# Performance work log

Measured on AMD Instinct MI355X. Metric: run time of the kernel, lower is better.

## Reference

```python
import jax, jax.numpy as jnp
import numpy as np

NUM_HEADS = 16

def setup_inputs() -> dict:
    key = jax.random.key(0)
    ks = jax.random.split(key, 12)
    B, NQ, NK = 4, 1024, 1024
    DQ = DK = DV = 1024
    AH = 1024   # num_heads * head_dim
    OUT = 1024
    s = lambda d: 1.0 / np.sqrt(d)
    return {
        "q": jax.random.normal(ks[0], (B, NQ, DQ), jnp.float32),
        "k": jax.random.normal(ks[1], (B, NK, DK), jnp.float32),
        "v": jax.random.normal(ks[2], (B, NK, DV), jnp.float32),
        "attn_mask": jnp.ones((NQ, NK), jnp.float32),
        "Wq": jax.random.normal(ks[3], (DQ, AH), jnp.float32) * s(DQ),
        "bq": jnp.zeros((AH,), jnp.float32),
        "Wk": jax.random.normal(ks[4], (DK, AH), jnp.float32) * s(DK),
        "bk": jnp.zeros((AH,), jnp.float32),
        "Wv": jax.random.normal(ks[5], (DV, AH), jnp.float32) * s(DV),
        "bv": jnp.zeros((AH,), jnp.float32),
        "Wo": jax.random.normal(ks[6], (AH, OUT), jnp.float32) * s(AH),
        "bo": jnp.zeros((OUT,), jnp.float32),
    }

def reference(q, k, v, attn_mask, Wq, bq, Wk, bk, Wv, bv, Wo, bo):
    b, n_q, _ = q.shape
    n_k = k.shape[1]
    all_head_dim = Wq.shape[1]
    scale = all_head_dim ** (-0.5)  # NOTE: module scales by all_head_dim, not head_dim

    # module reshapes as (b, n, head_dim, num_heads): heads are the LAST axis
    def split_heads(x):
        return x.reshape(b, x.shape[1], -1, NUM_HEADS).transpose(0, 3, 1, 2)  # (b,H,n,d)

    qh = split_heads(q @ Wq + bq) * scale
    kh = split_heads(k @ Wk + bk)
    vh = split_heads(v @ Wv + bv)

    attn = jnp.einsum('bhqd,bhkd->bhqk', qh, kh)
    attn = attn - 100000000.0 * (1.0 - attn_mask[None, None, :, :])
    attn = jax.nn.softmax(attn, axis=-1)

    o = jnp.einsum('bhqk,bhkd->bhqd', attn, vh)
    o = o.transpose(0, 2, 3, 1).reshape(b, n_q, -1)  # (b,n_q,head_dim*H)
    return o @ Wo + bo
```

## Files before the change

### kernel.cpp

```cpp
#include <hip/hip_runtime.h>
#include <stdint.h>

typedef __attribute__((ext_vector_type(8))) short short8;
typedef __attribute__((ext_vector_type(8))) unsigned short ushort8;
typedef __attribute__((ext_vector_type(4))) float f32x4;
typedef unsigned short u16;
typedef unsigned int u32;

__device__ __forceinline__ u16 f2bf(float f){
  u32 u = __builtin_bit_cast(u32, f);
  u32 r = (u + 0x7fffu + ((u >> 16) & 1u)) >> 16;
  return (u16)r;
}

__device__ __forceinline__ void gload16(const void* g, void* l){
  __builtin_amdgcn_global_load_lds((const __attribute__((address_space(1))) void*)g,
                                   (__attribute__((address_space(3))) void*)l, 16, 0, 0);
}

__global__ void cast3_kernel(const float* __restrict__ q, const float* __restrict__ k,
                             const float* __restrict__ v, u16* __restrict__ xq,
                             u16* __restrict__ xk, u16* __restrict__ xv){
  const int NV8 = 4194304 / 8;
  int stride = gridDim.x * blockDim.x;
  for (int i = blockIdx.x * blockDim.x + threadIdx.x; i < 3 * NV8; i += stride){
    int t = i / NV8, r = i - t * NV8;
    const float4* src = (const float4*)(t == 0 ? q : (t == 1 ? k : v));
    u16* dst = (t == 0 ? xq : (t == 1 ? xk : xv));
    float4 f0 = src[r * 2], f1 = src[r * 2 + 1];
    ushort8 o;
    o[0] = f2bf(f0.x); o[1] = f2bf(f0.y); o[2] = f2bf(f0.z); o[3] = f2bf(f0.w);
    o[4] = f2bf(f1.x); o[5] = f2bf(f1.y); o[6] = f2bf(f1.z); o[7] = f2bf(f1.w);
    *(ushort8*)(dst + r * 8) = o;
  }
}

__global__ void transw_kernel(const float* __restrict__ Wq, const float* __restrict__ Wk,
                              const float* __restrict__ Wv, const float* __restrict__ Wo,
                              u16* __restrict__ WqT, u16* __restrict__ WkT,
                              u16* __restrict__ WvT, u16* __restrict__ WoT){
  __shared__ float t[64][65];
  int z = blockIdx.z;
  const float* src = (z == 0 ? Wq : (z == 1 ? Wk : (z == 2 ? Wv : Wo)));
  u16* dst = (z == 0 ? WqT : (z == 1 ? WkT : (z == 2 ? WvT : WoT)));
  int tid = threadIdx.x;
  int bx = blockIdx.x, by = blockIdx.y;
  int c0 = by * 64;
  #pragma unroll
  for (int p = 0; p < 4; ++p){
    int rl = p * 16 + (tid >> 4);
    int srcRow = (z < 3) ? (bx * 64 + rl) : (rl * 16 + bx);
    float4 f = *(const float4*)(src + srcRow * 1024 + c0 + (tid & 15) * 4);
    t[rl][(tid & 15) * 4 + 0] = f.x;
    t[rl][(tid & 15) * 4 + 1] = f.y;
    t[rl][(tid & 15) * 4 + 2] = f.z;
    t[rl][(tid & 15) * 4 + 3] = f.w;
  }
  __syncthreads();
  int ro = tid >> 2;
  int kc = (tid & 3) * 16;
  int outBase = (c0 + ro) * 1024 + bx * 64;
  #pragma unroll
  for (int j = 0; j < 16; ++j)
    dst[outBase + kc + j] = f2bf(t[kc + j][ro]);
}

__global__ void maskflag_kernel(const float* __restrict__ mask, u32* __restrict__ flags){
  int q0 = blockIdx.x * 128, k0 = blockIdx.y * 64;
  int tid = threadIdx.x;
  bool ok = true;
  #pragma unroll
  for (int p = 0; p < 8; ++p){
    int fi = p * 256 + tid;
    int r = fi >> 4, c = (fi & 15) * 4;
    float4 f = *(const float4*)(mask + (size_t)(q0 + r) * 1024 + k0 + c);
    ok = ok && (f.x == 1.0f) && (f.y == 1.0f) && (f.z == 1.0f) && (f.w == 1.0f);
  }
  __shared__ int s_ok[4];
  unsigned long long b = __ballot(ok);
  if ((tid & 63) == 0) s_ok[tid >> 6] = (b == ~0ull) ? 1 : 0;
  __syncthreads();
  if (tid == 0)
    flags[blockIdx.x * 16 + blockIdx.y] = (u32)(s_ok[0] & s_ok[1] & s_ok[2] & s_ok[3]);
}

struct QkvArgs {
  const u16* A[3]; const u16* BT[3]; const float* bias[3];
  u16* outQ; u16* outK; u16* outVT;
};

__global__ __launch_bounds__(256, 4)
void gemm_qkv_kernel(QkvArgs args){
  __shared__ __align__(16) u16 As[2][128 * 32];
  __shared__ __align__(16) u16 Bs[2][128 * 32];
  int wg = blockIdx.x;
  int l  = (wg & 7) * 96 + (wg >> 3);
  int z  = l >> 8;
  int rem = l & 255;
  int m0 = (rem >> 3) * 128, n0 = (rem & 7) * 128;
  const u16* __restrict__ A  = args.A[z];
  const u16* __restrict__ BT = args.BT[z];
  const float* __restrict__ bias = args.bias[z];
  int tid = threadIdx.x, w = tid >> 6, lane = tid & 63, lr = lane & 15, lg = lane >> 4;
  int wr = w >> 1, wc = w & 1;
  f32x4 acc[4][4];
  #pragma unroll
  for (int i = 0; i < 4; ++i)
    #pragma unroll
    for (int j = 0; j < 4; ++j)
      acc[i][j] = f32x4{0.f, 0.f, 0.f, 0.f};

  auto stage = [&](int kt, int b){
    int k0 = kt * 32;
    #pragma unroll
    for (int p = 0; p < 2; ++p){
      int chunk = p * 4096 + w * 1024;
      int L = chunk + lane * 16;
      int row = L >> 6, inrow = L & 63;
      int srcB = inrow ^ (((row >> 1) & 3) << 4);
      gload16(A + (m0 + row) * 1024 + k0 + (srcB >> 1), (char*)As[b] + chunk);
      gload16(BT + (n0 + row) * 1024 + k0 + (srcB >> 1), (char*)Bs[b] + chunk);
    }
  };
  stage(0, 0);

  for (int kt = 0; kt < 32; ++kt){
    int cur = kt & 1;
    if (kt < 31){
      stage(kt + 1, cur ^ 1);
      asm volatile("s_waitcnt vmcnt(4)" ::: "memory");
    } else {
      asm volatile("s_waitcnt vmcnt(0)" ::: "memory");
    }
    __builtin_amdgcn_s_barrier();

    short8 af[4], bfr[4];
    int cb = lg * 16;
    #pragma unroll
    for (int i = 0; i < 4; ++i){
      int ra = wr * 64 + i * 16 + lr;
      af[i] = *(const short8*)((const char*)As[cur] + ra * 64 + (cb ^ (((ra >> 1) & 3) << 4)));
      int rb = wc * 64 + i * 16 + lr;
      bfr[i] = *(const short8*)((const char*)Bs[cur] + rb * 64 + (cb ^ (((rb >> 1) & 3) << 4)));
    }
    #pragma unroll
    for (int i = 0; i < 4; ++i)
      #pragma unroll
      for (int j = 0; j < 4; ++j)
        acc[i][j] = __builtin_amdgcn_mfma_f32_16x16x32_bf16(af[i], bfr[j], acc[i][j], 0, 0, 0);

    __builtin_amdgcn_s_barrier();
  }

  float bv[4];
  #pragma unroll
  for (int j = 0; j < 4; ++j) bv[j] = bias[n0 + wc * 64 + j * 16 + lr];
  float scale = (z == 0) ? 0.03125f : 1.0f;
  int bb = m0 >> 10;
  int dd0 = (n0 + wc * 64) >> 4;
  if (z == 2){
    #pragma unroll
    for (int i = 0; i < 4; ++i){
      int nn0 = (m0 + wr * 64 + i * 16 + lg * 4) & 1023;
      #pragma unroll
      for (int j = 0; j < 4; ++j){
        ushort4 pw;
        pw.x = f2bf((acc[i][j][0] + bv[j]) * scale);
        pw.y = f2bf((acc[i][j][1] + bv[j]) * scale);
        pw.z = f2bf((acc[i][j][2] + bv[j]) * scale);
        pw.w = f2bf((acc[i][j][3] + bv[j]) * scale);
        *(ushort4*)(args.outVT + ((size_t)(bb * 16 + lr) * 64 + dd0 + j) * 1024 + nn0) = pw;
      }
    }
  } else {
    u16* o = (z == 0) ? args.outQ : args.outK;
    #pragma unroll
    for (int i = 0; i < 4; ++i){
      #pragma unroll
      for (int rr = 0; rr < 4; ++rr){
        int nn = (m0 + wr * 64 + i * 16 + lg * 4 + rr) & 1023;
        ushort4 pw;
        pw.x = f2bf((acc[i][0][rr] + bv[0]) * scale);
        pw.y = f2bf((acc[i][1][rr] + bv[1]) * scale);
        pw.z = f2bf((acc[i][2][rr] + bv[2]) * scale);
        pw.w = f2bf((acc[i][3][rr] + bv[3]) * scale);
        *(ushort4*)(o + ((size_t)(bb * 16 + lr) * 1024 + nn) * 64 + dd0) = pw;
      }
    }
  }
}

__global__ __launch_bounds__(256, 2)
void attn_kernel(const u16* __restrict__ Qh, const u16* __restrict__ Kh,
                 const u16* __restrict__ VT, const float* __restrict__ mask,
                 const u32* __restrict__ flags, u16* __restrict__ Oh){
  __shared__ __align__(16) u16 Qs[128 * 64];
  __shared__ __align__(16) u16 Ks[2][64 * 64];
  __shared__ __align__(16) u16 Vs[2][64 * 64];
  __shared__ __align__(16) u16 Ps[128 * 72];
  int tid = threadIdx.x, w = tid >> 6, lane = tid & 63, lr = lane & 15, lg = lane >> 4;
  int wg = blockIdx.x;
  int idx = wg >> 3;
  int bh = (wg & 7) * 8 + (idx >> 3);
  int qt = idx & 7;
  int q0 = qt * 128;
  const u16* Qb = Qh + (size_t)bh * 65536;
  const u16* Kb = Kh + (size_t)bh * 65536;
  const u16* Vb = VT + (size_t)bh * 65536;

  u32 fbits = 0;
  #pragma unroll
  for (int t = 0; t < 16; ++t) fbits |= (flags[qt * 16 + t] & 1u) << t;

  #pragma unroll
  for (int r = 0; r < 4; ++r){
    int chunk = (r * 4 + w) * 1024;
    int L = chunk + lane * 16;
    int row = L >> 7, inrow = L & 127;
    int srcB = inrow ^ ((row & 7) << 4);
    gload16(Qb + (q0 + row) * 64 + (srcB >> 1), (char*)Qs + chunk);
  }

  auto stage_kv = [&](int t, int b){
    int kn = t * 64;
    #pragma unroll
    for (int r = 0; r < 2; ++r){
      int chunk = (r * 4 + w) * 1024;
      int L = chunk + lane * 16;
      int row = L >> 7, inrow = L & 127;
      int srcB = inrow ^ ((row & 7) << 4);
      gload16(Kb + (kn + row) * 64 + (srcB >> 1), (char*)Ks[b] + chunk);
      gload16(Vb + row * 1024 + kn + (srcB >> 1), (char*)Vs[b] + chunk);
    }
  };
  stage_kv(0, 0);

  f32x4 o[2][4];
  float m_run[2], l_run[2];
  m_run[0] = m_run[1] = -3.0e38f;
  l_run[0] = l_run[1] = 0.f;
  #pragma unroll
  for (int i = 0; i < 2; ++i)
    #pragma unroll
    for (int j = 0; j < 4; ++j)
      o[i][j] = f32x4{0.f, 0.f, 0.f, 0.f};

  for (int kt = 0; kt < 16; ++kt){
    int cur = kt & 1;
    int kn0 = kt * 64;

    f32x4 s[2][4];
    if (fbits & (1u << kt)){
      #pragma unroll
      for (int i = 0; i < 2; ++i)
        #pragma unroll
        for (int j = 0; j < 4; ++j)
          s[i][j] = f32x4{0.f, 0.f, 0.f, 0.f};
    } else {
      #pragma unroll
      for (int i = 0; i < 2; ++i){
        int qg = q0 + w * 32 + i * 16 + lr;
        #pragma unroll
        for (int j = 0; j < 4; ++j){
          int kg = kn0 + j * 16 + lg * 4;
          float4 mm = *(const float4*)(mask + (size_t)qg * 1024 + kg);
          s[i][j][0] = fmaf(100000000.0f, mm.x, -100000000.0f);
          s[i][j][1] = fmaf(100000000.0f, mm.y, -100000000.0f);
          s[i][j][2] = fmaf(100000000.0f, mm.z, -100000000.0f);
          s[i][j][3] = fmaf(100000000.0f, mm.w, -100000000.0f);
        }
      }
    }

    if (kt < 15){
      stage_kv(kt + 1, cur ^ 1);
      asm volatile("s_waitcnt vmcnt(4)" ::: "memory");
    } else {
      asm volatile("s_waitcnt vmcnt(0)" ::: "memory");
    }
    __builtin_amdgcn_s_barrier();

    #pragma unroll
    for (int kh = 0; kh < 2; ++kh){
      short8 qf[2], kf[4];
      int cb = kh * 64 + lg * 16;
      #pragma unroll
      for (int i = 0; i < 2; ++i){
        int ra = w * 32 + i * 16 + lr;
        qf[i] = *(const short8*)((const char*)Qs + ra * 128 + (cb ^ ((ra & 7) << 4)));
      }
      #pragma unroll
      for (int j = 0; j < 4; ++j){
        int rb = j * 16 + lr;
        kf[j] = *(const short8*)((const char*)Ks[cur] + rb * 128 + (cb ^ ((rb & 7) << 4)));
      }
      #pragma unroll
      for (int i = 0; i < 2; ++i)
        #pragma unroll
        for (int j = 0; j < 4; ++j)
          s[i][j] = __builtin_amdgcn_mfma_f32_16x16x32_bf16(kf[j], qf[i], s[i][j], 0, 0, 0);
    }

    float alpha[2];
    #pragma unroll
    for (int i = 0; i < 2; ++i){
      float m0a = fmaxf(fmaxf(s[i][0][0], s[i][0][1]), fmaxf(s[i][0][2], s[i][0][3]));
      float m1a = fmaxf(fmaxf(s[i][1][0], s[i][1][1]), fmaxf(s[i][1][2], s[i][1][3]));
      float m2a = fmaxf(fmaxf(s[i][2][0], s[i][2][1]), fmaxf(s[i][2][2], s[i][2][3]));
      float m3a = fmaxf(fmaxf(s[i][3][0], s[i][3][1]), fmaxf(s[i][3][2], s[i][3][3]));
      float mx = fmaxf(fmaxf(m0a, m1a), fmaxf(m2a, m3a));
      mx = fmaxf(mx, __shfl_xor(mx, 16));
      mx = fmaxf(mx, __shfl_xor(mx, 32));
      float mnew = fmaxf(m_run[i], mx);
      alpha[i] = __expf(m_run[i] - mnew);
      m_run[i] = mnew;
      float rs = 0.f;
      #pragma unroll
      for (int j = 0; j < 4; ++j)
        #pragma unroll
        for (int rr = 0; rr < 4; ++rr){
          float p = __expf(s[i][j][rr] - mnew);
          s[i][j][rr] = p;
          rs += p;
        }
      rs += __shfl_xor(rs, 16);
      rs += __shfl_xor(rs, 32);
      l_run[i] = l_run[i] * alpha[i] + rs;
      int prow = w * 32 + i * 16 + lr;
      #pragma unroll
      for (int j = 0; j < 4; ++j){
        ushort4 pw;
        pw.x = f2bf(s[i][j][0]); pw.y = f2bf(s[i][j][1]);
        pw.z = f2bf(s[i][j][2]); pw.w = f2bf(s[i][j][3]);
        *(ushort4*)(Ps + prow * 72 + j * 16 + lg * 4) = pw;
      }
    }

    #pragma unroll
    for (int i = 0; i < 2; ++i)
      #pragma unroll
      for (int jd = 0; jd < 4; ++jd)
        #pragma unroll
        for (int rr = 0; rr < 4; ++rr)
          o[i][jd][rr] *= alpha[i];

    #pragma unroll
    for (int kh = 0; kh < 2; ++kh){
      short8 pf[2], vf[4];
      int cb = kh * 64 + lg * 16;
      #pragma unroll
      for (int i = 0; i < 2; ++i){
        int ra = w * 32 + i * 16 + lr;
        pf[i] = *(const short8*)((const char*)Ps + ra * 144 + cb);
      }
      #pragma unroll
      for (int jd = 0; jd < 4; ++jd){
        int rb = jd * 16 + lr;
        vf[jd] = *(const short8*)((const char*)Vs[cur] + rb * 128 + (cb ^ ((rb & 7) << 4)));
      }
      #pragma unroll
      for (int i = 0; i < 2; ++i)
        #pragma unroll
        for (int jd = 0; jd < 4; ++jd)
          o[i][jd] = __builtin_amdgcn_mfma_f32_16x16x32_bf16(vf[jd], pf[i], o[i][jd], 0, 0, 0);
    }
    __builtin_amdgcn_s_barrier();
  }

  #pragma unroll
  for (int i = 0; i < 2; ++i){
    float inv = 1.0f / l_run[i];
    int qg = q0 + w * 32 + i * 16 + lr;
    #pragma unroll
    for (int jd = 0; jd < 4; ++jd){
      ushort4 ov;
      ov.x = f2bf(o[i][jd][0] * inv);
      ov.y = f2bf(o[i][jd][1] * inv);
      ov.z = f2bf(o[i][jd][2] * inv);
      ov.w = f2bf(o[i][jd][3] * inv);
      *(ushort4*)(Oh + ((size_t)bh * 1024 + qg) * 64 + jd * 16 + lg * 4) = ov;
    }
  }
}

__global__ __launch_bounds__(256, 4)
void gemm_out_kernel(const u16* __restrict__ Oh, const u16* __restrict__ WoT,
                     const float* __restrict__ bo, float* __restrict__ out){
  __shared__ __align__(16) u16 As[2][128 * 32];
  __shared__ __align__(16) u16 Bs[2][128 * 32];
  int wg = blockIdx.x;
  int l  = (wg & 7) * 32 + (wg >> 3);
  int m0 = (l >> 3) * 128, n0 = (l & 7) * 128;
  int tid = threadIdx.x, w = tid >> 6, lane = tid & 63, lr = lane & 15, lg = lane >> 4;
  int wr = w >> 1, wc = w & 1;
  f32x4 acc[4][4];
  #pragma unroll
  for (int i = 0; i < 4; ++i)
    #pragma unroll
    for (int j = 0; j < 4; ++j)
      acc[i][j] = f32x4{0.f, 0.f, 0.f, 0.f};

  auto stage = [&](int kt, int b){
    int hh = kt >> 1;
    int dofs = (kt & 1) * 32;
    int k0 = kt * 32;
    #pragma unroll
    for (int p = 0; p < 2; ++p){
      int chunk = p * 4096 + w * 1024;
      int L = chunk + lane * 16;
      int row = L >> 6, inrow = L & 63;
      int srcB = inrow ^ (((row >> 1) & 3) << 4);
      int m = m0 + row;
      int bb = m >> 10, nn = m & 1023;
      gload16(Oh + ((size_t)(bb * 16 + hh) * 1024 + nn) * 64 + dofs + (srcB >> 1),
              (char*)As[b] + chunk);
      gload16(WoT + (n0 + row) * 1024 + k0 + (srcB >> 1), (char*)Bs[b] + chunk);
    }
  };
  stage(0, 0);

  for (int kt = 0; kt < 32; ++kt){
    int cur = kt & 1;
    if (kt < 31){
      stage(kt + 1, cur ^ 1);
      asm volatile("s_waitcnt vmcnt(4)" ::: "memory");
    } else {
      asm volatile("s_waitcnt vmcnt(0)" ::: "memory");
    }
    __builtin_amdgcn_s_barrier();

    short8 af[4], bfr[4];
    int cb = lg * 16;
    #pragma unroll
    for (int i = 0; i < 4; ++i){
      int ra = wr * 64 + i * 16 + lr;
      af[i] = *(const short8*)((const char*)As[cur] + ra * 64 + (cb ^ (((ra >> 1) & 3) << 4)));
      int rb = wc * 64 + i * 16 + lr;
      bfr[i] = *(const short8*)((const char*)Bs[cur] + rb * 64 + (cb ^ (((rb >> 1) & 3) << 4)));
    }
    #pragma unroll
    for (int i = 0; i < 4; ++i)
      #pragma unroll
      for (int j = 0; j < 4; ++j)
        acc[i][j] = __builtin_amdgcn_mfma_f32_16x16x32_bf16(af[i], bfr[j], acc[i][j], 0, 0, 0);

    __builtin_amdgcn_s_barrier();
  }

  float bv[4];
  #pragma unroll
  for (int j = 0; j < 4; ++j) bv[j] = bo[n0 + wc * 64 + j * 16 + lr];
  #pragma unroll
  for (int i = 0; i < 4; ++i)
    #pragma unroll
    for (int j = 0; j < 4; ++j){
      int gcol = n0 + wc * 64 + j * 16 + lr;
      #pragma unroll
      for (int rr = 0; rr < 4; ++rr){
        int grow = m0 + wr * 64 + i * 16 + lg * 4 + rr;
        out[(size_t)grow * 1024 + gcol] = acc[i][j][rr] + bv[j];
      }
    }
}

extern "C" void kernel_launch(void* const* d_in, const int* in_sizes, int n_in,
                              void* d_out, int out_size, void* d_ws, size_t ws_size,
                              hipStream_t stream){
  const float* q    = (const float*)d_in[0];
  const float* k    = (const float*)d_in[1];
  const float* v    = (const float*)d_in[2];
  const float* mask = (const float*)d_in[3];
  const float* Wq   = (const float*)d_in[4];
  const float* bq   = (const float*)d_in[5];
  const float* Wk   = (const float*)d_in[6];
  const float* bk   = (const float*)d_in[7];
  const float* Wv   = (const float*)d_in[8];
  const float* bv   = (const float*)d_in[9];
  const float* Wo   = (const float*)d_in[10];
  const float* bo   = (const float*)d_in[11];

  char* ws = (char*)d_ws;
  u16* Qh  = (u16*)(ws + (size_t)0);
  u16* Kh  = (u16*)(ws + ((size_t)8  << 20));
  u16* VT  = (u16*)(ws + ((size_t)16 << 20));
  u16* Oh  = (u16*)(ws + ((size_t)24 << 20));
  u16* Xq  = (u16*)(ws + ((size_t)32 << 20));
  u16* Xk  = (u16*)(ws + ((size_t)40 << 20));
  u16* Xv  = (u16*)(ws + ((size_t)48 << 20));
  u16* WqT = (u16*)(ws + ((size_t)56 << 20));
  u16* WkT = (u16*)(ws + ((size_t)58 << 20));
  u16* WvT = (u16*)(ws + ((size_t)60 << 20));
  u16* WoT = (u16*)(ws + ((size_t)62 << 20));
  u32* Flags = (u32*)(ws + ((size_t)32 << 20));

  cast3_kernel<<<dim3(2048), dim3(256), 0, stream>>>(q, k, v, Xq, Xk, Xv);
  transw_kernel<<<dim3(16, 16, 4), dim3(256), 0, stream>>>(Wq, Wk, Wv, Wo, WqT, WkT, WvT, WoT);

  QkvArgs a;
  a.A[0] = Xq;  a.A[1] = Xk;  a.A[2] = Xv;
  a.BT[0] = WqT; a.BT[1] = WkT; a.BT[2] = WvT;
  a.bias[0] = bq; a.bias[1] = bk; a.bias[2] = bv;
  a.outQ = Qh; a.outK = Kh; a.outVT = VT;
  gemm_qkv_kernel<<<dim3(768), dim3(256), 0, stream>>>(a);

  maskflag_kernel<<<dim3(8, 16), dim3(256), 0, stream>>>(mask, Flags);
  attn_kernel<<<dim3(512), dim3(256), 0, stream>>>(Qh, Kh, VT, mask, Flags, Oh);
  gemm_out_kernel<<<dim3(256), dim3(256), 0, stream>>>(Oh, WoT, bo, (float*)d_out);
}
```

Before: 130.1 us.

## Triple-buffer GEMM loads, halve output GEMM tile width, merge prep kernels

```diff
diff --git a/kernel.cpp b/kernel.cpp
--- a/kernel.cpp
+++ b/kernel.cpp
@@ -18,51 +18,52 @@
                                    (__attribute__((address_space(3))) void*)l, 16, 0, 0);
 }
 
-__global__ void cast3_kernel(const float* __restrict__ q, const float* __restrict__ k,
-                             const float* __restrict__ v, u16* __restrict__ xq,
-                             u16* __restrict__ xk, u16* __restrict__ xv){
-  const int NV8 = 4194304 / 8;
-  int stride = gridDim.x * blockDim.x;
-  for (int i = blockIdx.x * blockDim.x + threadIdx.x; i < 3 * NV8; i += stride){
-    int t = i / NV8, r = i - t * NV8;
-    const float4* src = (const float4*)(t == 0 ? q : (t == 1 ? k : v));
-    u16* dst = (t == 0 ? xq : (t == 1 ? xk : xv));
-    float4 f0 = src[r * 2], f1 = src[r * 2 + 1];
-    ushort8 o;
-    o[0] = f2bf(f0.x); o[1] = f2bf(f0.y); o[2] = f2bf(f0.z); o[3] = f2bf(f0.w);
-    o[4] = f2bf(f1.x); o[5] = f2bf(f1.y); o[6] = f2bf(f1.z); o[7] = f2bf(f1.w);
-    *(ushort8*)(dst + r * 8) = o;
-  }
-}
-
-__global__ void transw_kernel(const float* __restrict__ Wq, const float* __restrict__ Wk,
-                              const float* __restrict__ Wv, const float* __restrict__ Wo,
-                              u16* __restrict__ WqT, u16* __restrict__ WkT,
-                              u16* __restrict__ WvT, u16* __restrict__ WoT){
+__global__ void prep_kernel(const float* __restrict__ q, const float* __restrict__ k,
+                            const float* __restrict__ v, u16* __restrict__ xq,
+                            u16* __restrict__ xk, u16* __restrict__ xv,
+                            const float* __restrict__ Wq, const float* __restrict__ Wk,
+                            const float* __restrict__ Wv, const float* __restrict__ Wo,
+                            u16* __restrict__ WqT, u16* __restrict__ WkT,
+                            u16* __restrict__ WvT, u16* __restrict__ WoT){
   __shared__ float t[64][65];
-  int z = blockIdx.z;
-  const float* src = (z == 0 ? Wq : (z == 1 ? Wk : (z == 2 ? Wv : Wo)));
-  u16* dst = (z == 0 ? WqT : (z == 1 ? WkT : (z == 2 ? WvT : WoT)));
+  int bid = blockIdx.x;
   int tid = threadIdx.x;
-  int bx = blockIdx.x, by = blockIdx.y;
-  int c0 = by * 64;
-  #pragma unroll
-  for (int p = 0; p < 4; ++p){
-    int rl = p * 16 + (tid >> 4);
-    int srcRow = (z < 3) ? (bx * 64 + rl) : (rl * 16 + bx);
-    float4 f = *(const float4*)(src + srcRow * 1024 + c0 + (tid & 15) * 4);
-    t[rl][(tid & 15) * 4 + 0] = f.x;
-    t[rl][(tid & 15) * 4 + 1] = f.y;
-    t[rl][(tid & 15) * 4 + 2] = f.z;
-    t[rl][(tid & 15) * 4 + 3] = f.w;
-  }
-  __syncthreads();
-  int ro = tid >> 2;
-  int kc = (tid & 3) * 16;
-  int outBase = (c0 + ro) * 1024 + bx * 64;
-  #pragma unroll
-  for (int j = 0; j < 16; ++j)
-    dst[outBase + kc + j] = f2bf(t[kc + j][ro]);
+  if (bid < 2048){
+    const int NV8 = 4194304 / 8;
+    for (int i = bid * 256 + tid; i < 3 * NV8; i += 2048 * 256){
+      int tt = i / NV8, r = i - tt * NV8;
+      const float4* src = (const float4*)(tt == 0 ? q : (tt == 1 ? k : v));
+      u16* dst = (tt == 0 ? xq : (tt == 1 ? xk : xv));
+      float4 f0 = src[r * 2], f1 = src[r * 2 + 1];
+      ushort8 o;
+      o[0] = f2bf(f0.x); o[1] = f2bf(f0.y); o[2] = f2bf(f0.z); o[3] = f2bf(f0.w);
+      o[4] = f2bf(f1.x); o[5] = f2bf(f1.y); o[6] = f2bf(f1.z); o[7] = f2bf(f1.w);
+      *(ushort8*)(dst + r * 8) = o;
+    }
+  } else {
+    int idx = bid - 2048;
+    int bx = idx & 15, by = (idx >> 4) & 15, z = idx >> 8;
+    const float* src = (z == 0 ? Wq : (z == 1 ? Wk : (z == 2 ? Wv : Wo)));
+    u16* dst = (z == 0 ? WqT : (z == 1 ? WkT : (z == 2 ? WvT : WoT)));
+    int c0 = by * 64;
+    #pragma unroll
+    for (int p = 0; p < 4; ++p){
+      int rl = p * 16 + (tid >> 4);
+      int srcRow = (z < 3) ? (bx * 64 + rl) : (rl * 16 + bx);
+      float4 f = *(const float4*)(src + srcRow * 1024 + c0 + (tid & 15) * 4);
+      t[rl][(tid & 15) * 4 + 0] = f.x;
+      t[rl][(tid & 15) * 4 + 1] = f.y;
+      t[rl][(tid & 15) * 4 + 2] = f.z;
+      t[rl][(tid & 15) * 4 + 3] = f.w;
+    }
+    __syncthreads();
+    int ro = tid >> 2;
+    int kc = (tid & 3) * 16;
+    int outBase = (c0 + ro) * 1024 + bx * 64;
+    #pragma unroll
+    for (int j = 0; j < 16; ++j)
+      dst[outBase + kc + j] = f2bf(t[kc + j][ro]);
+  }
 }
 
 __global__ void maskflag_kernel(const float* __restrict__ mask, u32* __restrict__ flags){
@@ -89,10 +90,10 @@
   u16* outQ; u16* outK; u16* outVT;
 };
 
-__global__ __launch_bounds__(256, 4)
+__global__ __launch_bounds__(256, 3)
 void gemm_qkv_kernel(QkvArgs args){
-  __shared__ __align__(16) u16 As[2][128 * 32];
-  __shared__ __align__(16) u16 Bs[2][128 * 32];
+  __shared__ __align__(16) u16 As[3][128 * 32];
+  __shared__ __align__(16) u16 Bs[3][128 * 32];
   int wg = blockIdx.x;
   int l  = (wg & 7) * 96 + (wg >> 3);
   int z  = l >> 8;
@@ -123,11 +124,14 @@
     }
   };
   stage(0, 0);
+  stage(1, 1);
 
   for (int kt = 0; kt < 32; ++kt){
-    int cur = kt & 1;
-    if (kt < 31){
-      stage(kt + 1, cur ^ 1);
+    int cur = kt % 3;
+    if (kt < 30){
+      stage(kt + 2, (kt + 2) % 3);
+      asm volatile("s_waitcnt vmcnt(8)" ::: "memory");
+    } else if (kt == 30){
       asm volatile("s_waitcnt vmcnt(4)" ::: "memory");
     } else {
       asm volatile("s_waitcnt vmcnt(0)" ::: "memory");
@@ -386,18 +390,18 @@
 __global__ __launch_bounds__(256, 4)
 void gemm_out_kernel(const u16* __restrict__ Oh, const u16* __restrict__ WoT,
                      const float* __restrict__ bo, float* __restrict__ out){
-  __shared__ __align__(16) u16 As[2][128 * 32];
-  __shared__ __align__(16) u16 Bs[2][128 * 32];
+  __shared__ __align__(16) u16 As[3][128 * 32];
+  __shared__ __align__(16) u16 Bs[3][64 * 32];
   int wg = blockIdx.x;
-  int l  = (wg & 7) * 32 + (wg >> 3);
-  int m0 = (l >> 3) * 128, n0 = (l & 7) * 128;
+  int l  = (wg & 7) * 64 + (wg >> 3);
+  int m0 = (l >> 4) * 128, n0 = (l & 15) * 64;
   int tid = threadIdx.x, w = tid >> 6, lane = tid & 63, lr = lane & 15, lg = lane >> 4;
-  int wr = w >> 1, wc = w & 1;
-  f32x4 acc[4][4];
+  int wm = w >> 1, wn = w & 1;
+  f32x4 acc[4][2];
   #pragma unroll
   for (int i = 0; i < 4; ++i)
     #pragma unroll
-    for (int j = 0; j < 4; ++j)
+    for (int j = 0; j < 2; ++j)
       acc[i][j] = f32x4{0.f, 0.f, 0.f, 0.f};
 
   auto stage = [&](int kt, int b){
@@ -414,50 +418,62 @@
       int bb = m >> 10, nn = m & 1023;
       gload16(Oh + ((size_t)(bb * 16 + hh) * 1024 + nn) * 64 + dofs + (srcB >> 1),
               (char*)As[b] + chunk);
+    }
+    {
+      int chunk = w * 1024;
+      int L = chunk + lane * 16;
+      int row = L >> 6, inrow = L & 63;
+      int srcB = inrow ^ (((row >> 1) & 3) << 4);
       gload16(WoT + (n0 + row) * 1024 + k0 + (srcB >> 1), (char*)Bs[b] + chunk);
     }
   };
   stage(0, 0);
+  stage(1, 1);
 
   for (int kt = 0; kt < 32; ++kt){
-    int cur = kt & 1;
-    if (kt < 31){
-      stage(kt + 1, cur ^ 1);
-      asm volatile("s_waitcnt vmcnt(4)" ::: "memory");
+    int cur = kt % 3;
+    if (kt < 30){
+      stage(kt + 2, (kt + 2) % 3);
+      asm volatile("s_waitcnt vmcnt(6)" ::: "memory");
+    } else if (kt == 30){
+      asm volatile("s_waitcnt vmcnt(3)" ::: "memory");
     } else {
       asm volatile("s_waitcnt vmcnt(0)" ::: "memory");
     }
     __builtin_amdgcn_s_barrier();
 
-    short8 af[4], bfr[4];
+    short8 af[4], bfr[2];
     int cb = lg * 16;
     #pragma unroll
     for (int i = 0; i < 4; ++i){
-      int ra = wr * 64 + i * 16 + lr;
+      int ra = wm * 64 + i * 16 + lr;
       af[i] = *(const short8*)((const char*)As[cur] + ra * 64 + (cb ^ (((ra >> 1) & 3) << 4)));
-      int rb = wc * 64 + i * 16 + lr;
-      bfr[i] = *(const short8*)((const char*)Bs[cur] + rb * 64 + (cb ^ (((rb >> 1) & 3) << 4)));
+    }
+    #pragma unroll
+    for (int j = 0; j < 2; ++j){
+      int rb = wn * 32 + j * 16 + lr;
+      bfr[j] = *(const short8*)((const char*)Bs[cur] + rb * 64 + (cb ^ (((rb >> 1) & 3) << 4)));
     }
     #pragma unroll
     for (int i = 0; i < 4; ++i)
       #pragma unroll
-      for (int j = 0; j < 4; ++j)
+      for (int j = 0; j < 2; ++j)
         acc[i][j] = __builtin_amdgcn_mfma_f32_16x16x32_bf16(af[i], bfr[j], acc[i][j], 0, 0, 0);
 
     __builtin_amdgcn_s_barrier();
   }
 
-  float bv[4];
-  #pragma unroll
-  for (int j = 0; j < 4; ++j) bv[j] = bo[n0 + wc * 64 + j * 16 + lr];
+  float bv[2];
+  #pragma unroll
+  for (int j = 0; j < 2; ++j) bv[j] = bo[n0 + wn * 32 + j * 16 + lr];
   #pragma unroll
   for (int i = 0; i < 4; ++i)
     #pragma unroll
-    for (int j = 0; j < 4; ++j){
-      int gcol = n0 + wc * 64 + j * 16 + lr;
+    for (int j = 0; j < 2; ++j){
+      int gcol = n0 + wn * 32 + j * 16 + lr;
       #pragma unroll
       for (int rr = 0; rr < 4; ++rr){
-        int grow = m0 + wr * 64 + i * 16 + lg * 4 + rr;
+        int grow = m0 + wm * 64 + i * 16 + lg * 4 + rr;
         out[(size_t)grow * 1024 + gcol] = acc[i][j][rr] + bv[j];
       }
     }
@@ -493,8 +509,8 @@
   u16* WoT = (u16*)(ws + ((size_t)62 << 20));
   u32* Flags = (u32*)(ws + ((size_t)32 << 20));
 
-  cast3_kernel<<<dim3(2048), dim3(256), 0, stream>>>(q, k, v, Xq, Xk, Xv);
-  transw_kernel<<<dim3(16, 16, 4), dim3(256), 0, stream>>>(Wq, Wk, Wv, Wo, WqT, WkT, WvT, WoT);
+  prep_kernel<<<dim3(3072), dim3(256), 0, stream>>>(q, k, v, Xq, Xk, Xv,
+                                                    Wq, Wk, Wv, Wo, WqT, WkT, WvT, WoT);
 
   QkvArgs a;
   a.A[0] = Xq;  a.A[1] = Xk;  a.A[2] = Xv;
@@ -505,5 +521,5 @@
 
   maskflag_kernel<<<dim3(8, 16), dim3(256), 0, stream>>>(mask, Flags);
   attn_kernel<<<dim3(512), dim3(256), 0, stream>>>(Qh, Kh, VT, mask, Flags, Oh);
-  gemm_out_kernel<<<dim3(256), dim3(256), 0, stream>>>(Oh, WoT, bo, (float*)d_out);
-}
+  gemm_out_kernel<<<dim3(512), dim3(256), 0, stream>>>(Oh, WoT, bo, (float*)d_out);
+}
```

Result: faster. 125.4 us (-3.6%).
